# Optimization experiments

Hardware: AMD Instinct MI355X
Metric: run time of the kernel (lower is better)

## Reference

```python
import math
import jax, jax.numpy as jnp
import numpy as np

B, T, S, H, L, NH = 2, 512, 2048, 768, 32, 12
INTERMED = 4 * H


def _make_pe(max_len, hidden):
    position = np.arange(max_len)[:, None].astype(np.float32)
    div_term = np.exp(np.arange(0, hidden, 2).astype(np.float32) * (-math.log(10000.0) / hidden))
    pe = np.zeros((max_len, hidden), dtype=np.float32)
    pe[:, 0::2] = np.sin(position * div_term)
    pe[:, 1::2] = np.cos(position * div_term)
    return jnp.asarray(pe)


def setup_inputs() -> dict:
    key = jax.random.key(0)
    ks = jax.random.split(key, 10)
    token_reps = jax.random.normal(ks[0], (B, T, H), dtype=jnp.float32)
    starts = jax.random.randint(ks[1], (B, S), 0, T - L)
    lens = jax.random.randint(ks[2], (B, S), 1, L + 1)
    span_ids = jnp.stack([starts, starts + lens], axis=-1)  # (B,S,2)
    span_masks = jax.random.uniform(ks[3], (B, S)) > 0.2
    pe = _make_pe(T, H)
    dummy_query = jax.random.normal(ks[4], (H,), dtype=jnp.float32) * 0.02
    in_proj_w = jax.random.normal(ks[5], (3 * H, H), dtype=jnp.float32) * 0.02
    in_proj_b = jnp.zeros((3 * H,), jnp.float32)
    out_proj_w = jax.random.normal(ks[6], (H, H), dtype=jnp.float32) * 0.02
    out_proj_b = jnp.zeros((H,), jnp.float32)
    norm_g = jnp.ones((H,), jnp.float32)
    norm_b = jnp.zeros((H,), jnp.float32)
    ffn_w1 = jax.random.normal(ks[7], (INTERMED, H), dtype=jnp.float32) * (math.sqrt(2.0 / H))
    ffn_b1 = jnp.zeros((INTERMED,), jnp.float32)
    ffn_w2 = jax.random.normal(ks[8], (H, INTERMED), dtype=jnp.float32) * (math.sqrt(2.0 / INTERMED))
    ffn_b2 = jnp.zeros((H,), jnp.float32)
    return dict(token_reps=token_reps, span_ids=span_ids, span_masks=span_masks,
                pooling=0, pe=pe, dummy_query=dummy_query,
                in_proj_w=in_proj_w, in_proj_b=in_proj_b,
                out_proj_w=out_proj_w, out_proj_b=out_proj_b,
                norm_g=norm_g, norm_b=norm_b,
                ffn_w1=ffn_w1, ffn_b1=ffn_b1, ffn_w2=ffn_w2, ffn_b2=ffn_b2)


def _layernorm(x, g, b, eps=1e-5):
    mu = jnp.mean(x, axis=-1, keepdims=True)
    var = jnp.mean(jnp.square(x - mu), axis=-1, keepdims=True)
    return (x - mu) * jax.lax.rsqrt(var + eps) * g + b


def reference(token_reps, span_ids, span_masks, pooling, pe, dummy_query,
              in_proj_w, in_proj_b, out_proj_w, out_proj_b,
              norm_g, norm_b, ffn_w1, ffn_b1, ffn_w2, ffn_b2):
    b, t, h = token_reps.shape
    s = span_ids.shape[1]
    hd = h // NH
    # positional encoding over the sequence (dropout=0 / eval mode)
    x = token_reps + pe[:t]
    # ragged -> padded gather of span tokens
    starts = span_ids[..., 0]
    lens = (span_ids[..., 1] - starts) * span_masks.astype(span_ids.dtype)  # (B,S)
    ar = jnp.arange(L)
    pos = starts[..., None] + ar                     # (B,S,L)
    valid = ar[None, None, :] < lens[..., None]      # (B,S,L) True = real token
    idx = jnp.clip(pos, 0, t - 1)
    gathered = jax.vmap(lambda xb, ib: xb[ib])(x, idx)   # (B,S,L,H)
    gathered = gathered * valid[..., None]
    # guard fully-masked rows (masked-out / zero-len spans): keep one key valid,
    # output is zeroed at the end anyway (matches torch span_reps[~mask]=0)
    any_v = jnp.any(valid, axis=-1)
    valid = valid.at[..., 0].set(valid[..., 0] | ~any_v)
    # single-query multi-head attention (torch nn.MultiheadAttention math)
    Wq, Wk, Wv = jnp.split(in_proj_w, 3, axis=0)
    bq, bk, bv = jnp.split(in_proj_b, 3, axis=0)
    q = (dummy_query @ Wq.T + bq).reshape(NH, hd)                  # (NH,hd)
    k = (gathered @ Wk.T + bk).reshape(b, s, L, NH, hd)
    v = (gathered @ Wv.T + bv).reshape(b, s, L, NH, hd)
    scores = jnp.einsum('nd,bslnd->bsnl', q, k) / math.sqrt(hd)    # (B,S,NH,L)
    scores = jnp.where(valid[:, :, None, :], scores, -jnp.inf)
    attn = jax.nn.softmax(scores, axis=-1)
    ctx = jnp.einsum('bsnl,bslnd->bsnd', attn, v).reshape(b, s, h)
    attn_out = ctx @ out_proj_w.T + out_proj_b
    # residual + LayerNorm, FFN, residual + same LayerNorm
    x1 = _layernorm(attn_out + dummy_query, norm_g, norm_b)
    ffn = jax.nn.relu(x1 @ ffn_w1.T + ffn_b1) @ ffn_w2.T + ffn_b2
    out = _layernorm(ffn + x1, norm_g, norm_b)
    out = out * span_masks[..., None]
    return out
```

## Files before the change

### kernel.cpp

```cpp
#include <hip/hip_runtime.h>
#include <math.h>

static constexpr int B_  = 2;
static constexpr int T_  = 512;
static constexpr int S_  = 2048;
static constexpr int H_  = 768;
static constexpr int L_  = 32;
static constexpr int NH_ = 12;
static constexpr int HD_ = 64;
static constexpr int IM_ = 3072;

typedef __bf16 bf16x8 __attribute__((ext_vector_type(8)));
typedef float  f32x4  __attribute__((ext_vector_type(4)));

__device__ __forceinline__ float bf2f(unsigned short u) {
    return __uint_as_float(((unsigned)u) << 16);
}
__device__ __forceinline__ unsigned short f2bf(float f) {
    unsigned u = __float_as_uint(f);
    u += 0x7fffu + ((u >> 16) & 1u);
    return (unsigned short)(u >> 16);
}
__device__ __forceinline__ void gl_lds16(const void* g, void* l) {
    __builtin_amdgcn_global_load_lds((const __attribute__((address_space(1))) void*)g,
                                     (__attribute__((address_space(3))) void*)l, 16, 0, 0);
}

__global__ void k_q(const float* __restrict__ dq, const float* __restrict__ w,
                    const float* __restrict__ b, float* __restrict__ q,
                    const int* __restrict__ raw, int* __restrict__ mout) {
    int wv = threadIdx.x >> 6, lane = threadIdx.x & 63;
    int i = blockIdx.x * 4 + wv;
    const float* row = w + (size_t)i * H_;
    float acc = 0.f;
#pragma unroll
    for (int k = 0; k < 12; ++k) acc += dq[lane + 64 * k] * row[lane + 64 * k];
    for (int m = 32; m; m >>= 1) acc += __shfl_xor(acc, m, 64);
    if (lane == 0) q[i] = acc + b[i];
    if (blockIdx.x == 0) {
        __shared__ int bad;
        if (threadIdx.x == 0) bad = 0;
        __syncthreads();
        for (int t = threadIdx.x; t < 1024; t += 256) {
            int v = raw[t];
            if (v != 0 && v != 1) bad = 1;
        }
        __syncthreads();
        int byte_layout = bad;
        const unsigned char* rb = (const unsigned char*)raw;
        for (int t = threadIdx.x; t < B_ * S_; t += 256)
            mout[t] = byte_layout ? (int)rb[t] : raw[t];
    }
}

static constexpr int CWB = 2880;
__global__ void k_castw(const float* __restrict__ s0, const float* __restrict__ s1,
                        const float* __restrict__ s2, const float* __restrict__ s3,
                        unsigned short* __restrict__ d0, unsigned short* __restrict__ d1,
                        unsigned short* __restrict__ d2, unsigned short* __restrict__ d3,
                        const float* __restrict__ q, const float* __restrict__ wk,
                        float* __restrict__ wq) {
    if (blockIdx.x >= CWB) {
        int i = (blockIdx.x - CWB) * 256 + threadIdx.x;
        int n = i / H_, hh = i % H_;
        float acc = 0.f;
        for (int d = 0; d < HD_; ++d)
            acc += q[n * HD_ + d] * wk[(size_t)(H_ + n * HD_ + d) * H_ + hh];
        wq[i] = acc;
        return;
    }
    const long n0 = (long)H_ * H_, n2 = (long)IM_ * H_;
    long gid = (long)(blockIdx.x * 256 + threadIdx.x) * 8;
    const float* s; unsigned short* d; long off;
    if (gid < n0)                { s = s0; d = d0; off = gid; }
    else if (gid < 2 * n0)       { s = s1; d = d1; off = gid - n0; }
    else if (gid < 2 * n0 + n2)  { s = s2; d = d2; off = gid - 2 * n0; }
    else                         { s = s3; d = d3; off = gid - 2 * n0 - n2; }
    float4 f0 = *(const float4*)(s + off);
    float4 f1 = *(const float4*)(s + off + 4);
    uint4 o;
    o.x = (unsigned)f2bf(f0.x) | ((unsigned)f2bf(f0.y) << 16);
    o.y = (unsigned)f2bf(f0.z) | ((unsigned)f2bf(f0.w) << 16);
    o.z = (unsigned)f2bf(f1.x) | ((unsigned)f2bf(f1.y) << 16);
    o.w = (unsigned)f2bf(f1.z) | ((unsigned)f2bf(f1.w) << 16);
    *(uint4*)(d + off) = o;
}

__global__ void k_xstok(const float* __restrict__ tr, const float* __restrict__ pe,
                        const float* __restrict__ wq,
                        unsigned short* __restrict__ xbf, float* __restrict__ stok) {
    __shared__ float sx[H_];
    int bt = blockIdx.x, tid = threadIdx.x;
    const float* trow = tr + (size_t)bt * H_;
    const float* prow = pe + (size_t)(bt % T_) * H_;
    if (tid < 192) {
        int h0 = tid * 4;
        float4 a = *(const float4*)(trow + h0);
        float4 p = *(const float4*)(prow + h0);
        float v0 = a.x + p.x, v1 = a.y + p.y, v2 = a.z + p.z, v3 = a.w + p.w;
        sx[h0] = v0; sx[h0 + 1] = v1; sx[h0 + 2] = v2; sx[h0 + 3] = v3;
        uint2 o;
        o.x = (unsigned)f2bf(v0) | ((unsigned)f2bf(v1) << 16);
        o.y = (unsigned)f2bf(v2) | ((unsigned)f2bf(v3) << 16);
        *(uint2*)(xbf + (size_t)bt * H_ + h0) = o;
    }
    __syncthreads();
    int lane = tid & 63, w = tid >> 6;
    float xv[12];
#pragma unroll
    for (int k = 0; k < 12; ++k) xv[k] = sx[lane + 64 * k];
#pragma unroll
    for (int hh = 0; hh < 3; ++hh) {
        int n = w * 3 + hh;
        const float* wr = wq + (size_t)n * H_;
        float acc = 0.f;
#pragma unroll
        for (int k = 0; k < 12; ++k) acc += xv[k] * wr[lane + 64 * k];
        for (int m = 32; m; m >>= 1) acc += __shfl_xor(acc, m, 64);
        if (lane == 0) stok[bt * NH_ + n] = acc;
    }
}

__global__ void k_castv4(const unsigned short* __restrict__ p, size_t pstr,
                         unsigned short* __restrict__ dst, int n) {
    int i = (blockIdx.x * 256 + threadIdx.x) * 8;
    if (i >= n) return;
    float a[8] = {};
#pragma unroll
    for (int z = 0; z < 4; ++z) {
        uint4 u = *(const uint4*)(p + z * pstr + i);
        a[0] += bf2f((unsigned short)(u.x & 0xffff));
        a[1] += bf2f((unsigned short)(u.x >> 16));
        a[2] += bf2f((unsigned short)(u.y & 0xffff));
        a[3] += bf2f((unsigned short)(u.y >> 16));
        a[4] += bf2f((unsigned short)(u.z & 0xffff));
        a[5] += bf2f((unsigned short)(u.z >> 16));
        a[6] += bf2f((unsigned short)(u.w & 0xffff));
        a[7] += bf2f((unsigned short)(u.w >> 16));
    }
    uint4 o;
    o.x = (unsigned)f2bf(a[0]) | ((unsigned)f2bf(a[1]) << 16);
    o.y = (unsigned)f2bf(a[2]) | ((unsigned)f2bf(a[3]) << 16);
    o.z = (unsigned)f2bf(a[4]) | ((unsigned)f2bf(a[5]) << 16);
    o.w = (unsigned)f2bf(a[6]) | ((unsigned)f2bf(a[7]) << 16);
    *(uint4*)(dst + i) = o;
}

template <bool RELU, bool SPLIT>
__global__ __launch_bounds__(256)
void gemm_bt(const unsigned short* __restrict__ A, const unsigned short* __restrict__ W,
             const float* __restrict__ bias, unsigned short* __restrict__ Cout,
             int M, int N, int K, int kLen, int TX, int SP) {
    __shared__ unsigned short As[4096];
    __shared__ unsigned short Bs[4096];
    const int qx = blockIdx.x & 7, t = blockIdx.x >> 3;
    const int gi = t / TX, x = t - gi * TX;
    const int g = gi * 8 + qx;
    int y, z;
    if (SPLIT) { y = g / SP; z = g - y * SP; } else { y = g; z = 0; }
    const int bm = y * 128, bn = x * 128;
    const int kOff = z * kLen;

    const int tid = threadIdx.x, lane = tid & 63, wid = tid >> 6;
    const int wm = (wid >> 1) * 64, wn = (wid & 1) * 64;
    const int r16 = lane >> 2, c4 = lane & 3;
    const int swc = (c4 ^ ((r16 >> 1) & 3)) * 8;
    const unsigned short* agp = A + (size_t)(bm + wid * 32 + r16) * K + kOff + swc;
    const unsigned short* bgp = W + (size_t)(bn + wid * 32 + r16) * K + kOff + swc;
    unsigned short* lA = As + wid * 1024;
    unsigned short* lB = Bs + wid * 1024;

    f32x4 acc[4][4];
#pragma unroll
    for (int i = 0; i < 4; ++i)
#pragma unroll
        for (int j = 0; j < 4; ++j) acc[i][j] = f32x4{0.f, 0.f, 0.f, 0.f};

    const int mrow = lane & 15;
    const int q4 = lane >> 4;
    const int sw = (q4 ^ ((mrow >> 1) & 3)) * 8;
    const int NIT = kLen >> 5;

    for (int it = 0; it < NIT; ++it) {
        const int k0 = it << 5;
        gl_lds16(agp + k0, lA);
        gl_lds16(agp + (size_t)16 * K + k0, lA + 512);
        gl_lds16(bgp + k0, lB);
        gl_lds16(bgp + (size_t)16 * K + k0, lB + 512);
        __syncthreads();
        bf16x8 af[4], bfr[4];
#pragma unroll
        for (int i = 0; i < 4; ++i)
            af[i] = *(const bf16x8*)(As + (wm + i * 16 + mrow) * 32 + sw);
#pragma unroll
        for (int j = 0; j < 4; ++j)
            bfr[j] = *(const bf16x8*)(Bs + (wn + j * 16 + mrow) * 32 + sw);
#pragma unroll
        for (int i = 0; i < 4; ++i)
#pragma unroll
            for (int j = 0; j < 4; ++j)
                acc[i][j] = __builtin_amdgcn_mfma_f32_16x16x32_bf16(af[i], bfr[j], acc[i][j], 0, 0, 0);
        __syncthreads();
    }

    const bool addb = !SPLIT || z == 0;
    unsigned short* outp = SPLIT ? Cout + (size_t)z * M * N : Cout;
    const int lr = (lane >> 4) * 4, lc = lane & 15;
#pragma unroll
    for (int j = 0; j < 4; ++j) {
        int col = bn + wn + j * 16 + lc;
        float bv = addb ? bias[col] : 0.f;
#pragma unroll
        for (int i = 0; i < 4; ++i) {
            int row0 = bm + wm + i * 16 + lr;
#pragma unroll
            for (int r = 0; r < 4; ++r) {
                float v = acc[i][j][r] + bv;
                if (RELU) v = fmaxf(v, 0.f);
                outp[(size_t)(row0 + r) * N + col] = f2bf(v);
            }
        }
    }
}

#define STG(gp_, lp_, h_, kt_) do {                                           \
    const unsigned short* _g = (gp_) + (size_t)((h_) * 128) * K + (kt_) * 64; \
    unsigned short* _l = (lp_) + (h_) * (128 * 64);                           \
    gl_lds16(_g, _l);                                                         \
    gl_lds16(_g + (size_t)8 * K, _l + 8 * 64);                                \
} while (0)

#define LDF(dst_, mat_, rowoff_, kk_)                                         \
    dst_ = *(const bf16x8*)((const char*)(mat_) + (rowoff_) * 128 + rbase +   \
                            ((kk_) ? c1 : c0))

#define RD_A(mat_, base_) do {                                                \
    LDF(a_[0][0], mat_, (base_) + 0,  0); LDF(a_[0][1], mat_, (base_) + 0,  1); \
    LDF(a_[1][0], mat_, (base_) + 16, 0); LDF(a_[1][1], mat_, (base_) + 16, 1); \
    LDF(a_[2][0], mat_, (base_) + 32, 0); LDF(a_[2][1], mat_, (base_) + 32, 1); \
    LDF(a_[3][0], mat_, (base_) + 48, 0); LDF(a_[3][1], mat_, (base_) + 48, 1); \
} while (0)

#define RD_B(dst_, mat_, base_) do {                                          \
    LDF(dst_[0][0], mat_, (base_) + 0,  0); LDF(dst_[0][1], mat_, (base_) + 0,  1); \
    LDF(dst_[1][0], mat_, (base_) + 16, 0); LDF(dst_[1][1], mat_, (base_) + 16, 1); \
} while (0)

#define QPH(MH_, NH_, B_) do {                                                \
    _Pragma("unroll")                                                         \
    for (int m_ = 0; m_ < 4; ++m_) {                                          \
        _Pragma("unroll")                                                     \
        for (int n_ = 0; n_ < 2; ++n_) {                                      \
            f32x4 c_ = acc[(MH_) * 4 + m_][(NH_) * 2 + n_];                   \
            c_ = __builtin_amdgcn_mfma_f32_16x16x32_bf16(a_[m_][0], B_[n_][0], c_, 0, 0, 0); \
            c_ = __builtin_amdgcn_mfma_f32_16x16x32_bf16(a_[m_][1], B_[n_][1], c_, 0, 0, 0); \
            acc[(MH_) * 4 + m_][(NH_) * 2 + n_] = c_;                         \
        }                                                                     \
    }                                                                         \
} while (0)

#define PH_MID do {                                                           \
    __builtin_amdgcn_s_barrier();                                             \
    asm volatile("s_waitcnt lgkmcnt(0)" ::: "memory");                        \
    __builtin_amdgcn_sched_barrier(0);                                        \
    __builtin_amdgcn_s_setprio(1);                                            \
} while (0)

#define PH_END do {                                                           \
    __builtin_amdgcn_s_setprio(0);                                            \
    __builtin_amdgcn_s_barrier();                                             \
    __builtin_amdgcn_sched_barrier(0);                                        \
} while (0)

#define PH_ENDV do {                                                          \
    __builtin_amdgcn_s_setprio(0);                                            \
    asm volatile("s_waitcnt vmcnt(4)" ::: "memory");                          \
    __builtin_amdgcn_s_barrier();                                             \
    __builtin_amdgcn_sched_barrier(0);                                        \
} while (0)

template <bool RELU, bool SPLIT>
__global__ __launch_bounds__(512)
void gemm256(const unsigned short* __restrict__ A, const unsigned short* __restrict__ W,
             const float* __restrict__ bias, unsigned short* __restrict__ Cout,
             int M, int N, int K, int kLen, int NTt, int SP) {
    __shared__ unsigned short lds[4][256 * 64];
    (void)SP;
    const int MT = M >> 8;
    int bid = blockIdx.x;
    int z = 0, rem = bid;
    if (SPLIT) { int tpz = MT * NTt; z = bid / tpz; rem = bid - z * tpz; }
    const int y = rem / NTt, x = rem - y * NTt;
    const int bm = y * 256, bn = x * 256;
    const int kOff = z * kLen;
    const int NT = kLen >> 6;
    const int NIT2 = NT >> 1;

    const int tid = threadIdx.x, lane = tid & 63, wid = tid >> 6;
    const int wm = (wid >> 2) * 128, wn = (wid & 3) * 64;
    const int mrow = lane & 15, q4 = lane >> 4;
    const int rbase = mrow * 128;
    const int c0 = (q4 ^ (mrow & 7)) * 16;
    const int c1 = ((4 + q4) ^ (mrow & 7)) * 16;

    const int srow = wid * 16 + (lane >> 3);
    const int gcol = ((lane & 7) ^ ((lane >> 3) & 7)) * 8;
    const unsigned short* agp = A + (size_t)(bm + srow) * K + kOff + gcol;
    const unsigned short* bgp = W + (size_t)(bn + srow) * K + kOff + gcol;
    unsigned short* const aLp0 = lds[0] + wid * 1024;
    unsigned short* const bLp0 = lds[1] + wid * 1024;
    unsigned short* const aLp1 = lds[2] + wid * 1024;
    unsigned short* const bLp1 = lds[3] + wid * 1024;

    f32x4 acc[8][4];
#pragma unroll
    for (int i = 0; i < 8; ++i)
#pragma unroll
        for (int j = 0; j < 4; ++j) acc[i][j] = f32x4{0.f, 0.f, 0.f, 0.f};

    bf16x8 a_[4][2], b0_[2][2], b1_[2][2];

    STG(agp, aLp0, 0, 0);
    STG(agp, aLp0, 1, 0);
    STG(bgp, bLp0, 0, 0);
    STG(bgp, bLp0, 1, 0);
    STG(bgp, bLp1, 0, 1);
    STG(agp, aLp1, 0, 1);
    asm volatile("s_waitcnt vmcnt(4)" ::: "memory");
    __builtin_amdgcn_s_barrier();
    __builtin_amdgcn_sched_barrier(0);

    for (int t = 0; t < NIT2; ++t) {
        const int k1 = 2 * t + 1;
        int k2 = 2 * t + 2; if (k2 > NT - 1) k2 = NT - 1;
        int k3 = 2 * t + 3; if (k3 > NT - 1) k3 = NT - 1;
        RD_A(lds[0], wm);
        RD_B(b0_, lds[1], wn);
        STG(bgp, bLp1, 1, k1);
        PH_MID; QPH(0, 0, b0_); PH_END;
        RD_B(b1_, lds[1], wn + 32);
        STG(agp, aLp1, 1, k1);
        PH_MID; QPH(0, 1, b1_); PH_END;
        RD_A(lds[0], wm + 64);
        STG(bgp, bLp0, 0, k2);
        PH_MID; QPH(1, 0, b0_); PH_END;
        STG(agp, aLp0, 0, k2);
        PH_MID; QPH(1, 1, b1_); PH_ENDV;
        RD_A(lds[2], wm);
        RD_B(b0_, lds[3], wn);
        STG(bgp, bLp0, 1, k2);
        PH_MID; QPH(0, 0, b0_); PH_END;
        RD_B(b1_, lds[3], wn + 32);
        STG(agp, aLp0, 1, k2);
        PH_MID; QPH(0, 1, b1_); PH_END;
        RD_A(lds[2], wm + 64);
        STG(bgp, bLp1, 0, k3);
        PH_MID; QPH(1, 0, b0_); PH_END;
        STG(agp, aLp1, 0, k3);
        PH_MID; QPH(1, 1, b1_); PH_ENDV;
    }

    const bool addb = !SPLIT || z == 0;
    unsigned short* outp = SPLIT ? Cout + (size_t)z * M * N : Cout;
    const int lr = (lane >> 4) * 4, lc = lane & 15;
#pragma unroll
    for (int j = 0; j < 4; ++j) {
        int col = bn + wn + j * 16 + lc;
        float bv = addb ? bias[col] : 0.f;
#pragma unroll
        for (int i = 0; i < 8; ++i) {
            int row0 = bm + wm + i * 16 + lr;
#pragma unroll
            for (int r = 0; r < 4; ++r) {
                float v = acc[i][j][r] + bv;
                if (RELU) v = fmaxf(v, 0.f);
                outp[(size_t)(row0 + r) * N + col] = f2bf(v);
            }
        }
    }
}

__global__ void k_attn(const float* __restrict__ stok, const unsigned short* __restrict__ vtok,
                       const int* __restrict__ span_ids, const int* __restrict__ masks,
                       unsigned short* __restrict__ ctx) {
    int r = blockIdx.x, b = r / S_;
    unsigned short* out = ctx + (size_t)r * H_;
    int tid = threadIdx.x;
    __shared__ float w[NH_][L_];
    __shared__ int idxs[L_];
    __shared__ int s_len;
    if (tid == 0) {
        int m = masks[r];
        int st = span_ids[2 * r], en = span_ids[2 * r + 1];
        int len = m ? (en - st) : 0;
        len = len < 0 ? 0 : (len > L_ ? L_ : len);
        s_len = len;
    }
    __syncthreads();
    int len = s_len;
    if (len == 0) {
        for (int h2 = tid; h2 < H_ / 2; h2 += 256) ((unsigned*)out)[h2] = 0u;
        return;
    }
    if (tid < L_) {
        int p = span_ids[2 * r] + tid;
        idxs[tid] = p < 0 ? 0 : (p > T_ - 1 ? T_ - 1 : p);
    }
    __syncthreads();
    for (int i = tid; i < NH_ * L_; i += 256) {
        int n = i / L_, l = i % L_;
        w[n][l] = (l < len) ? stok[(size_t)(b * T_ + idxs[l]) * NH_ + n] * 0.125f : -INFINITY;
    }
    __syncthreads();
    if (tid < NH_) {
        float mx = -INFINITY;
        for (int l = 0; l < len; ++l) mx = fmaxf(mx, w[tid][l]);
        float sum = 0.f;
        for (int l = 0; l < len; ++l) { float e = __expf(w[tid][l] - mx); w[tid][l] = e; sum += e; }
        float inv = 1.f / sum;
        for (int l = 0; l < len; ++l) w[tid][l] *= inv;
    }
    __syncthreads();
    if (tid < 192) {
        int h0 = tid * 4, n = h0 >> 6;
        float a0 = 0.f, a1 = 0.f, a2 = 0.f, a3 = 0.f;
        for (int l = 0; l < len; ++l) {
            float wl = w[n][l];
            const unsigned short* vr = vtok + (size_t)(b * T_ + idxs[l]) * H_ + h0;
            uint2 u = *(const uint2*)vr;
            a0 += wl * bf2f((unsigned short)(u.x & 0xffff));
            a1 += wl * bf2f((unsigned short)(u.x >> 16));
            a2 += wl * bf2f((unsigned short)(u.y & 0xffff));
            a3 += wl * bf2f((unsigned short)(u.y >> 16));
        }
        uint2 o;
        o.x = (unsigned)f2bf(a0) | ((unsigned)f2bf(a1) << 16);
        o.y = (unsigned)f2bf(a2) | ((unsigned)f2bf(a3) << 16);
        *(uint2*)(out + h0) = o;
    }
}

template <bool RESROW, bool MASKOUT>
__global__ void k_ln(const unsigned short* __restrict__ parts, size_t pstr,
                     const float* __restrict__ resf, const unsigned short* __restrict__ resb,
                     const float* __restrict__ g, const float* __restrict__ bt,
                     float* __restrict__ outf, unsigned short* __restrict__ outb,
                     const int* __restrict__ masks) {
    int r = blockIdx.x;
    int tid = threadIdx.x;
    float v[3];
    float lsum = 0.f;
#pragma unroll
    for (int i = 0; i < 3; ++i) {
        int h = tid + 256 * i;
        float s = RESROW ? bf2f(resb[(size_t)r * H_ + h]) : resf[h];
#pragma unroll
        for (int z = 0; z < 4; ++z)
            s += bf2f(parts[z * pstr + (size_t)r * H_ + h]);
        v[i] = s;
        lsum += s;
    }
    __shared__ float sh[256];
    sh[tid] = lsum;
    __syncthreads();
    for (int st = 128; st > 0; st >>= 1) {
        if (tid < st) sh[tid] += sh[tid + st];
        __syncthreads();
    }
    float mean = sh[0] * (1.f / H_);
    __syncthreads();
    float lvar = 0.f;
#pragma unroll
    for (int i = 0; i < 3; ++i) { float d = v[i] - mean; lvar += d * d; }
    sh[tid] = lvar;
    __syncthreads();
    for (int st = 128; st > 0; st >>= 1) {
        if (tid < st) sh[tid] += sh[tid + st];
        __syncthreads();
    }
    float var = sh[0] * (1.f / H_);
    float scale = rsqrtf(var + 1e-5f);
    float mfac = 1.f;
    if (MASKOUT) mfac = masks[r] ? 1.f : 0.f;
#pragma unroll
    for (int i = 0; i < 3; ++i) {
        int h = tid + 256 * i;
        float o = ((v[i] - mean) * scale * g[h] + bt[h]) * mfac;
        if (MASKOUT) outf[(size_t)r * H_ + h] = o;
        else         outb[(size_t)r * H_ + h] = f2bf(o);
    }
}

extern "C" void kernel_launch(void* const* d_in, const int* in_sizes, int n_in,
                              void* d_out, int out_size, void* d_ws, size_t ws_size,
                              hipStream_t stream) {
    const float* token_reps = (const float*)d_in[0];
    const int*   span_ids   = (const int*)d_in[1];
    const int*   masks_raw  = (const int*)d_in[2];
    const float* pe   = (const float*)d_in[4];
    const float* dq   = (const float*)d_in[5];
    const float* in_w = (const float*)d_in[6];
    const float* in_b = (const float*)d_in[7];
    const float* ow   = (const float*)d_in[8];
    const float* ob   = (const float*)d_in[9];
    const float* g    = (const float*)d_in[10];
    const float* bt   = (const float*)d_in[11];
    const float* w1   = (const float*)d_in[12];
    const float* b1   = (const float*)d_in[13];
    const float* w2   = (const float*)d_in[14];
    const float* b2   = (const float*)d_in[15];

    const int BS = B_ * S_;
    const int BT = B_ * T_;

    float* fws   = (float*)d_ws;
    float* stok  = fws;
    float* qv    = stok + BT * NH_;
    float* wqeff = qv + H_;
    unsigned short* us = (unsigned short*)(wqeff + NH_ * H_);
    unsigned short* pbuf = us;
    unsigned short* xbf  = pbuf + (size_t)4 * BS * H_;
    unsigned short* vtok = xbf + (size_t)BT * H_;
    unsigned short* ctx  = vtok + (size_t)BT * H_;
    unsigned short* x1bf = ctx + (size_t)BS * H_;
    unsigned short* f1   = x1bf + (size_t)BS * H_;
    unsigned short* wvb  = f1 + (size_t)BS * IM_;
    unsigned short* owb  = wvb + H_ * H_;
    unsigned short* w1b  = owb + H_ * H_;
    unsigned short* w2b  = w1b + IM_ * H_;
    int* maskn = (int*)(w2b + H_ * IM_);

    k_q<<<H_ / 4, 256, 0, stream>>>(dq, in_w, in_b, qv, masks_raw, maskn);
    k_castw<<<CWB + 36, 256, 0, stream>>>(
        in_w + (size_t)2 * H_ * H_, ow, w1, w2, wvb, owb, w1b, w2b,
        qv, in_w, wqeff);
    k_xstok<<<BT, 256, 0, stream>>>(token_reps, pe, wqeff, xbf, stok);
    gemm_bt<false, true><<<192, 256, 0, stream>>>(
        xbf, wvb, in_b + 2 * H_, pbuf, BT, H_, H_, H_ / 4, 6, 4);
    k_castv4<<<(BT * H_ / 8 + 255) / 256, 256, 0, stream>>>(
        pbuf, (size_t)BT * H_, vtok, BT * H_);
    k_attn<<<BS, 256, 0, stream>>>(stok, vtok, span_ids, maskn, ctx);
    gemm_bt<false, true><<<768, 256, 0, stream>>>(
        ctx, owb, ob, pbuf, BS, H_, H_, H_ / 4, 6, 4);
    k_ln<false, false><<<BS, 256, 0, stream>>>(
        pbuf, (size_t)BS * H_, dq, nullptr, g, bt, nullptr, x1bf, nullptr);
    gemm256<true, false><<<192, 512, 0, stream>>>(
        x1bf, w1b, b1, f1, BS, IM_, H_, H_, IM_ / 256, 1);
    gemm256<false, true><<<192, 512, 0, stream>>>(
        f1, w2b, b2, pbuf, BS, H_, IM_, IM_ / 4, H_ / 256, 4);
    k_ln<true, true><<<BS, 256, 0, stream>>>(
        pbuf, (size_t)BS * H_, nullptr, x1bf, g, bt, (float*)d_out, nullptr, maskn);
}
```

Baseline: 244.3 us.

## Double-buffer LDS in 128-tile GEMM and use it for FFN1

The 128x128 bf16 GEMM gains a two-stage LDS ring, so the global-to-LDS copy of the next K slice is issued before the current slice's MFMAs, with explicit vmcnt/lgkmcnt waits and raw barriers in place of __syncthreads. FFN1 moves from the 256x256 8-wave kernel to this double-buffered 128x128 kernel with 768 blocks. Templates are replaced by named per-GEMM kernels, and a final vmcnt(0) wait is added. The extra LDS doubles the footprint per block, and the last iteration issues a redundant load of the final slice.

```diff
diff --git a/kernel.cpp b/kernel.cpp
--- a/kernel.cpp
+++ b/kernel.cpp
@@ -146,13 +146,20 @@
     *(uint4*)(dst + i) = o;
 }
 
+#define STG2(c_, k0e_) do {                                                   \
+    gl_lds16(agp + (k0e_), lA + (c_) * 4096);                                 \
+    gl_lds16(agp + (size_t)16 * K + (k0e_), lA + (c_) * 4096 + 512);          \
+    gl_lds16(bgp + (k0e_), lB + (c_) * 4096);                                 \
+    gl_lds16(bgp + (size_t)16 * K + (k0e_), lB + (c_) * 4096 + 512);          \
+} while (0)
+
 template <bool RELU, bool SPLIT>
-__global__ __launch_bounds__(256)
-void gemm_bt(const unsigned short* __restrict__ A, const unsigned short* __restrict__ W,
-             const float* __restrict__ bias, unsigned short* __restrict__ Cout,
-             int M, int N, int K, int kLen, int TX, int SP) {
-    __shared__ unsigned short As[4096];
-    __shared__ unsigned short Bs[4096];
+__device__ __forceinline__
+void gemm_db_body(const unsigned short* __restrict__ A, const unsigned short* __restrict__ W,
+                  const float* __restrict__ bias, unsigned short* __restrict__ Cout,
+                  int M, int N, int K, int kLen, int TX, int SP) {
+    __shared__ unsigned short As[2][4096];
+    __shared__ unsigned short Bs[2][4096];
     const int qx = blockIdx.x & 7, t = blockIdx.x >> 3;
     const int gi = t / TX, x = t - gi * TX;
     const int g = gi * 8 + qx;
@@ -167,8 +174,8 @@
     const int swc = (c4 ^ ((r16 >> 1) & 3)) * 8;
     const unsigned short* agp = A + (size_t)(bm + wid * 32 + r16) * K + kOff + swc;
     const unsigned short* bgp = W + (size_t)(bn + wid * 32 + r16) * K + kOff + swc;
-    unsigned short* lA = As + wid * 1024;
-    unsigned short* lB = Bs + wid * 1024;
+    unsigned short* lA = &As[0][0] + wid * 1024;
+    unsigned short* lB = &Bs[0][0] + wid * 1024;
 
     f32x4 acc[4][4];
 #pragma unroll
@@ -181,27 +188,34 @@
     const int sw = (q4 ^ ((mrow >> 1) & 3)) * 8;
     const int NIT = kLen >> 5;
 
+    STG2(0, 0);
     for (int it = 0; it < NIT; ++it) {
-        const int k0 = it << 5;
-        gl_lds16(agp + k0, lA);
-        gl_lds16(agp + (size_t)16 * K + k0, lA + 512);
-        gl_lds16(bgp + k0, lB);
-        gl_lds16(bgp + (size_t)16 * K + k0, lB + 512);
-        __syncthreads();
+        const int cur = it & 1;
+        int nk = it + 1; if (nk >= NIT) nk = NIT - 1;
+        STG2(cur ^ 1, nk << 5);
+        asm volatile("s_waitcnt vmcnt(4)" ::: "memory");
+        __builtin_amdgcn_s_barrier();
+        __builtin_amdgcn_sched_barrier(0);
+        const unsigned short* Ac = &As[cur][0];
+        const unsigned short* Bc = &Bs[cur][0];
         bf16x8 af[4], bfr[4];
 #pragma unroll
         for (int i = 0; i < 4; ++i)
-            af[i] = *(const bf16x8*)(As + (wm + i * 16 + mrow) * 32 + sw);
+            af[i] = *(const bf16x8*)(Ac + (wm + i * 16 + mrow) * 32 + sw);
 #pragma unroll
         for (int j = 0; j < 4; ++j)
-            bfr[j] = *(const bf16x8*)(Bs + (wn + j * 16 + mrow) * 32 + sw);
+            bfr[j] = *(const bf16x8*)(Bc + (wn + j * 16 + mrow) * 32 + sw);
+        asm volatile("s_waitcnt lgkmcnt(0)" ::: "memory");
+        __builtin_amdgcn_sched_barrier(0);
 #pragma unroll
         for (int i = 0; i < 4; ++i)
 #pragma unroll
             for (int j = 0; j < 4; ++j)
                 acc[i][j] = __builtin_amdgcn_mfma_f32_16x16x32_bf16(af[i], bfr[j], acc[i][j], 0, 0, 0);
-        __syncthreads();
-    }
+        __builtin_amdgcn_s_barrier();
+        __builtin_amdgcn_sched_barrier(0);
+    }
+    asm volatile("s_waitcnt vmcnt(0)" ::: "memory");
 
     const bool addb = !SPLIT || z == 0;
     unsigned short* outp = SPLIT ? Cout + (size_t)z * M * N : Cout;
@@ -221,6 +235,22 @@
             }
         }
     }
+}
+
+__global__ __launch_bounds__(256)
+void g2_vtok(const unsigned short* A, const unsigned short* W, const float* bias,
+             unsigned short* Cout, int M, int N, int K, int kLen, int TX, int SP) {
+    gemm_db_body<false, true>(A, W, bias, Cout, M, N, K, kLen, TX, SP);
+}
+__global__ __launch_bounds__(256)
+void g2_oproj(const unsigned short* A, const unsigned short* W, const float* bias,
+              unsigned short* Cout, int M, int N, int K, int kLen, int TX, int SP) {
+    gemm_db_body<false, true>(A, W, bias, Cout, M, N, K, kLen, TX, SP);
+}
+__global__ __launch_bounds__(256)
+void g2_ffn1(const unsigned short* A, const unsigned short* W, const float* bias,
+             unsigned short* Cout, int M, int N, int K, int kLen, int TX, int SP) {
+    gemm_db_body<true, false>(A, W, bias, Cout, M, N, K, kLen, TX, SP);
 }
 
 #define STG(gp_, lp_, h_, kt_) do {                                           \
@@ -279,11 +309,11 @@
     __builtin_amdgcn_sched_barrier(0);                                        \
 } while (0)
 
-template <bool RELU, bool SPLIT>
 __global__ __launch_bounds__(512)
-void gemm256(const unsigned short* __restrict__ A, const unsigned short* __restrict__ W,
+void g8_ffn2(const unsigned short* __restrict__ A, const unsigned short* __restrict__ W,
              const float* __restrict__ bias, unsigned short* __restrict__ Cout,
              int M, int N, int K, int kLen, int NTt, int SP) {
+    constexpr bool RELU = false, SPLIT = true;
     __shared__ unsigned short lds[4][256 * 64];
     (void)SP;
     const int MT = M >> 8;
@@ -359,6 +389,7 @@
         STG(agp, aLp1, 0, k3);
         PH_MID; QPH(1, 1, b1_); PH_ENDV;
     }
+    asm volatile("s_waitcnt vmcnt(0)" ::: "memory");
 
     const bool addb = !SPLIT || z == 0;
     unsigned short* outp = SPLIT ? Cout + (size_t)z * M * N : Cout;
@@ -535,19 +566,19 @@
         in_w + (size_t)2 * H_ * H_, ow, w1, w2, wvb, owb, w1b, w2b,
         qv, in_w, wqeff);
     k_xstok<<<BT, 256, 0, stream>>>(token_reps, pe, wqeff, xbf, stok);
-    gemm_bt<false, true><<<192, 256, 0, stream>>>(
+    g2_vtok<<<192, 256, 0, stream>>>(
         xbf, wvb, in_b + 2 * H_, pbuf, BT, H_, H_, H_ / 4, 6, 4);
     k_castv4<<<(BT * H_ / 8 + 255) / 256, 256, 0, stream>>>(
         pbuf, (size_t)BT * H_, vtok, BT * H_);
     k_attn<<<BS, 256, 0, stream>>>(stok, vtok, span_ids, maskn, ctx);
-    gemm_bt<false, true><<<768, 256, 0, stream>>>(
+    g2_oproj<<<768, 256, 0, stream>>>(
         ctx, owb, ob, pbuf, BS, H_, H_, H_ / 4, 6, 4);
     k_ln<false, false><<<BS, 256, 0, stream>>>(
         pbuf, (size_t)BS * H_, dq, nullptr, g, bt, nullptr, x1bf, nullptr);
-    gemm256<true, false><<<192, 512, 0, stream>>>(
-        x1bf, w1b, b1, f1, BS, IM_, H_, H_, IM_ / 256, 1);
-    gemm256<false, true><<<192, 512, 0, stream>>>(
-        f1, w2b, b2, pbuf, BS, H_, IM_, IM_ / 4, H_ / 256, 4);
+    g2_ffn1<<<768, 256, 0, stream>>>(
+        x1bf, w1b, b1, f1, BS, IM_, H_, H_, 24, 1);
+    g8_ffn2<<<192, 512, 0, stream>>>(
+        f1, w2b, b2, pbuf, BS, H_, IM_, IM_ / 4, 3, 4);
     k_ln<true, true><<<BS, 256, 0, stream>>>(
         pbuf, (size_t)BS * H_, nullptr, x1bf, g, bt, (float*)d_out, nullptr, maskn);
 }
```

Measured after the change: 243.8 us. No clear change (-0.2%).
